# Kernel optimization log

Hardware: AMD Instinct MI355X
Metric: run time of the kernel (lower is better)

Reference implementation:

```python
import jax, jax.numpy as jnp
import numpy as np

GROUP_SIZE = 128

def setup_inputs() -> dict:
    key = jax.random.key(0)
    k1, k2, k3, k4, k5 = jax.random.split(key, 5)
    B, S, IN, OUT = 4, 2048, 4096, 4096
    G = IN // GROUP_SIZE  # 32 groups
    x = jax.random.normal(k1, (B, S, IN), dtype=jnp.float32)
    qweight = jax.random.randint(k2, (OUT, IN // 2), 0, 256, dtype=jnp.int32)
    scales = jax.random.uniform(k3, (OUT, G), dtype=jnp.float32) * 0.01 + 1e-4
    zeros = jax.random.randint(k4, (OUT, G), 0, 16, dtype=jnp.int32)
    bias = jax.random.normal(k5, (OUT,), dtype=jnp.float32) * 0.01
    return {"x": x, "qweight": qweight, "scales": scales, "zeros": zeros, "bias": bias}

def reference(x, qweight, scales, zeros, bias):
    out_f, half = qweight.shape
    in_f = half * 2
    G = scales.shape[1]
    # Unpack two 4-bit values per byte: low nibble at even index, high at odd.
    low = (qweight & 15).astype(x.dtype)
    high = ((qweight >> 4) & 15).astype(x.dtype)
    w = jnp.stack([low, high], axis=-1).reshape(out_f, in_f)  # interleaved [w0,w1,w2,...]
    # Groupwise dequant: (q - zero) * scale
    w = w.reshape(out_f, G, GROUP_SIZE)
    w = (w - zeros[:, :, None].astype(x.dtype)) * scales[:, :, None].astype(x.dtype)
    w = w.reshape(out_f, in_f)
    # Dense linear: y = x @ W^T + b
    out = jnp.einsum('bsi,oi->bso', x, w) + bias
    return out
```

## Files before the change

kernel.cpp:

```cpp
#include <hip/hip_runtime.h>
#include <hip/hip_bf16.h>

typedef __attribute__((ext_vector_type(4))) float f32x4;
typedef __attribute__((ext_vector_type(8))) short bf16x8;
typedef __attribute__((ext_vector_type(4))) int i32x4;

#define GS 128

#define GLOAD_LDS16(g, l)                                                        \
    __builtin_amdgcn_global_load_lds(                                            \
        (const __attribute__((address_space(1))) void*)(g),                      \
        (__attribute__((address_space(3))) void*)(l), 16, 0, 0)

__device__ __forceinline__ short f2bf(float f) {
    union { float f; unsigned u; } v; v.f = f;
    unsigned r = v.u + 0x7fffu + ((v.u >> 16) & 1u);
    return (short)(r >> 16);
}

__global__ void prep_kernel(const int* __restrict__ QW,
                            const float* __restrict__ SC,
                            const int* __restrict__ ZR,
                            const float* __restrict__ X,
                            signed char* __restrict__ W8,
                            float* __restrict__ WS,
                            signed char* __restrict__ Xq,
                            float* __restrict__ XS,
                            int N, int K, int G) {
    const int tid = threadIdx.x;
    const int lane = tid & 63;
    const int wid = tid >> 6;
    __shared__ float red[4];

    if ((int)blockIdx.x < N) {
        const int o = blockIdx.x;
        const int g = tid / 8;
        const float s = SC[(long)o * G + g];
        const float z = (float)ZR[(long)o * G + g];
        const int* p = QW + (long)o * (K / 2) + tid * 8;
        int v[8];
#pragma unroll
        for (int j = 0; j < 8; ++j) v[j] = p[j];
        float w[16];
#pragma unroll
        for (int j = 0; j < 8; ++j) {
            w[2 * j]     = ((float)(v[j] & 15) - z) * s;
            w[2 * j + 1] = ((float)((v[j] >> 4) & 15) - z) * s;
        }
        float am = 0.f;
#pragma unroll
        for (int j = 0; j < 16; ++j) am = fmaxf(am, fabsf(w[j]));
#pragma unroll
        for (int off = 32; off >= 1; off >>= 1) am = fmaxf(am, __shfl_xor(am, off));
        if (lane == 0) red[wid] = am;
        __syncthreads();
        float wmax = fmaxf(fmaxf(red[0], red[1]), fmaxf(red[2], red[3]));
        wmax = fmaxf(wmax, 1e-30f);
        const float qs = 127.0f / wmax;
        int out[4];
#pragma unroll
        for (int j = 0; j < 4; ++j) {
            int b0 = ((int)rintf(w[4 * j]     * qs)) & 255;
            int b1 = ((int)rintf(w[4 * j + 1] * qs)) & 255;
            int b2 = ((int)rintf(w[4 * j + 2] * qs)) & 255;
            int b3 = ((int)rintf(w[4 * j + 3] * qs)) & 255;
            out[j] = b0 | (b1 << 8) | (b2 << 16) | (b3 << 24);
        }
        *(i32x4*)(W8 + (long)o * K + tid * 16) = *(i32x4*)out;
        if (tid == 0) WS[o] = wmax / 127.0f;
    } else {
        const int row = blockIdx.x - N;
        const float* px = X + (long)row * K + tid * 16;
        f32x4 v[4];
#pragma unroll
        for (int j = 0; j < 4; ++j) v[j] = *(const f32x4*)(px + j * 4);
        float am = 0.f;
#pragma unroll
        for (int j = 0; j < 4; ++j)
#pragma unroll
            for (int i = 0; i < 4; ++i) am = fmaxf(am, fabsf(v[j][i]));
#pragma unroll
        for (int off = 32; off >= 1; off >>= 1) am = fmaxf(am, __shfl_xor(am, off));
        if (lane == 0) red[wid] = am;
        __syncthreads();
        float amax = fmaxf(fmaxf(red[0], red[1]), fmaxf(red[2], red[3]));
        amax = fmaxf(amax, 1e-30f);
        const float qs = 127.0f / amax;
        int out[4];
#pragma unroll
        for (int j = 0; j < 4; ++j) {
            int b0 = ((int)rintf(v[j][0] * qs)) & 255;
            int b1 = ((int)rintf(v[j][1] * qs)) & 255;
            int b2 = ((int)rintf(v[j][2] * qs)) & 255;
            int b3 = ((int)rintf(v[j][3] * qs)) & 255;
            out[j] = b0 | (b1 << 8) | (b2 << 16) | (b3 << 24);
        }
        *(i32x4*)(Xq + (long)row * K + tid * 16) = *(i32x4*)out;
        if (tid == 0) XS[row] = amax / 127.0f;
    }
}

__global__ __launch_bounds__(512, 2)
void gemm_i8_kernel(const signed char* __restrict__ A,
                    const signed char* __restrict__ B,
                    const float* __restrict__ WS,
                    const float* __restrict__ XS,
                    const float* __restrict__ BI,
                    float* __restrict__ Y,
                    int M, int N, int K) {
    extern __shared__ char smem[];

    const int tid = threadIdx.x;
    const int lane = tid & 63;
    const int wid = tid >> 6;
    const int wr = wid >> 2;
    const int wc = wid & 3;
    const int fr = lane & 15;
    const int fq = lane >> 4;

    const int nbn = N / 256;
    const int bid = blockIdx.x;
    const int cpx = gridDim.x >> 3;
    const int wgid = (bid & 7) * cpx + (bid >> 3);
    const int tm = wgid / nbn;
    const int tn = wgid % nbn;
    const long m0 = (long)tm * 256;
    const long n0 = (long)tn * 256;

    const int srow = wid * 8 + (lane >> 3);
    const int schunk = (lane & 7) ^ (lane >> 3);
    const signed char* gA = A + (m0 + srow) * (long)K + schunk * 16;
    const signed char* gB = B + (n0 + srow) * (long)K + schunk * 16;

    auto stageA = [&](int c2, int i, int kt) {
        GLOAD_LDS16(gA + (long)i * 64 * K + (long)kt * 128,
                    smem + c2 * 32768 + i * 8192 + wid * 1024);
    };
    auto stageB = [&](int b3, int i, int kt) {
        GLOAD_LDS16(gB + (long)i * 64 * K + (long)kt * 128,
                    smem + 65536 + b3 * 32768 + i * 8192 + wid * 1024);
    };

    const int rswz = fr & 7;

    i32x4 acc[8][4] = {};
    i32x4 bfr[4][2];
    i32x4 afr[4];

    const int NT = K / 128;

    stageB(0, 0, 0); stageB(0, 1, 0); stageB(0, 2, 0); stageB(0, 3, 0);
    stageA(0, 0, 0); stageA(0, 1, 0); stageA(0, 2, 0); stageA(0, 3, 0);
    stageB(1, 0, 1); stageB(1, 1, 1); stageB(1, 2, 1); stageB(1, 3, 1);
    asm volatile("s_waitcnt vmcnt(4)" ::: "memory");
    __builtin_amdgcn_s_barrier();

    for (int t = 0; t < NT - 2; ++t) {
        const char* sA = smem + (t & 1) * 32768;
        const char* sB = smem + 65536 + (t % 3) * 32768;
        const int nxtA = (t & 1) ^ 1;
        const int b2 = (t + 2) % 3;
#pragma unroll
        for (int ph = 0; ph < 4; ++ph) {
            const int ks = ph & 1;
            const int mh = ph >> 1;
#pragma unroll
            for (int mf = 0; mf < 4; ++mf) {
                int row = wr * 128 + mh * 64 + mf * 16 + fr;
                afr[mf] = *(const i32x4*)(sA + row * 128 + ((fq + 4 * ks) ^ rswz) * 16);
            }
            if (mh == 0) {
#pragma unroll
                for (int nf = 0; nf < 4; ++nf) {
                    int row = wc * 64 + nf * 16 + fr;
                    bfr[nf][ks] = *(const i32x4*)(sB + row * 128 + ((fq + 4 * ks) ^ rswz) * 16);
                }
            }
            if (ph == 0)      { stageA(nxtA, 0, t + 1); stageA(nxtA, 2, t + 1); }
            else if (ph == 1) { stageA(nxtA, 1, t + 1); stageA(nxtA, 3, t + 1); }
            else if (ph == 2) { stageB(b2, 0, t + 2); stageB(b2, 1, t + 2); }
            else              { stageB(b2, 2, t + 2); stageB(b2, 3, t + 2); }

            __builtin_amdgcn_s_setprio(1);
#pragma unroll
            for (int mf = 0; mf < 4; ++mf)
#pragma unroll
                for (int nf = 0; nf < 4; ++nf)
                    acc[mh * 4 + mf][nf] = __builtin_amdgcn_mfma_i32_16x16x64_i8(
                        afr[mf], bfr[nf][ks], acc[mh * 4 + mf][nf], 0, 0, 0);
            __builtin_amdgcn_s_setprio(0);
        }
        asm volatile("s_waitcnt vmcnt(4)" ::: "memory");
        __builtin_amdgcn_s_barrier();
    }

    {
        const int t = NT - 2;
        const char* sA = smem + (t & 1) * 32768;
        const char* sB = smem + 65536 + (t % 3) * 32768;
        const int nxtA = (t & 1) ^ 1;
#pragma unroll
        for (int ph = 0; ph < 4; ++ph) {
            const int ks = ph & 1;
            const int mh = ph >> 1;
#pragma unroll
            for (int mf = 0; mf < 4; ++mf) {
                int row = wr * 128 + mh * 64 + mf * 16 + fr;
                afr[mf] = *(const i32x4*)(sA + row * 128 + ((fq + 4 * ks) ^ rswz) * 16);
            }
            if (mh == 0) {
#pragma unroll
                for (int nf = 0; nf < 4; ++nf) {
                    int row = wc * 64 + nf * 16 + fr;
                    bfr[nf][ks] = *(const i32x4*)(sB + row * 128 + ((fq + 4 * ks) ^ rswz) * 16);
                }
            }
            if (ph == 0)      { stageA(nxtA, 0, t + 1); stageA(nxtA, 2, t + 1); }
            else if (ph == 1) { stageA(nxtA, 1, t + 1); stageA(nxtA, 3, t + 1); }

            __builtin_amdgcn_s_setprio(1);
#pragma unroll
            for (int mf = 0; mf < 4; ++mf)
#pragma unroll
                for (int nf = 0; nf < 4; ++nf)
                    acc[mh * 4 + mf][nf] = __builtin_amdgcn_mfma_i32_16x16x64_i8(
                        afr[mf], bfr[nf][ks], acc[mh * 4 + mf][nf], 0, 0, 0);
            __builtin_amdgcn_s_setprio(0);
        }
        asm volatile("s_waitcnt vmcnt(0)" ::: "memory");
        __builtin_amdgcn_s_barrier();
    }

    {
        const int t = NT - 1;
        const char* sA = smem + (t & 1) * 32768;
        const char* sB = smem + 65536 + (t % 3) * 32768;
#pragma unroll
        for (int ph = 0; ph < 4; ++ph) {
            const int ks = ph & 1;
            const int mh = ph >> 1;
#pragma unroll
            for (int mf = 0; mf < 4; ++mf) {
                int row = wr * 128 + mh * 64 + mf * 16 + fr;
                afr[mf] = *(const i32x4*)(sA + row * 128 + ((fq + 4 * ks) ^ rswz) * 16);
            }
            if (mh == 0) {
#pragma unroll
                for (int nf = 0; nf < 4; ++nf) {
                    int row = wc * 64 + nf * 16 + fr;
                    bfr[nf][ks] = *(const i32x4*)(sB + row * 128 + ((fq + 4 * ks) ^ rswz) * 16);
                }
            }
            __builtin_amdgcn_s_setprio(1);
#pragma unroll
            for (int mf = 0; mf < 4; ++mf)
#pragma unroll
                for (int nf = 0; nf < 4; ++nf)
                    acc[mh * 4 + mf][nf] = __builtin_amdgcn_mfma_i32_16x16x64_i8(
                        afr[mf], bfr[nf][ks], acc[mh * 4 + mf][nf], 0, 0, 0);
            __builtin_amdgcn_s_setprio(0);
        }
    }

#pragma unroll
    for (int nf = 0; nf < 4; ++nf) {
        const long col = n0 + wc * 64 + nf * 16 + fr;
        const float ws = WS[col];
        const float bv = BI[col];
#pragma unroll
        for (int m = 0; m < 8; ++m) {
            const long rbase = m0 + wr * 128 + (m >> 2) * 64 + (m & 3) * 16 + 4 * fq;
#pragma unroll
            for (int i = 0; i < 4; ++i)
                Y[(rbase + i) * N + col] =
                    (float)acc[m][nf][i] * (XS[rbase + i] * ws) + bv;
        }
    }
}

#define BM 128
#define BN 128
#define BK 64
#define PK 72

__global__ void gptq_gemm_fallback(const float* __restrict__ X,
                                   const int* __restrict__ QW,
                                   const float* __restrict__ SC,
                                   const int* __restrict__ ZR,
                                   const float* __restrict__ BI,
                                   float* __restrict__ Y,
                                   int M, int N, int K, int G) {
    __shared__ __align__(16) short As[BM * PK];
    __shared__ __align__(16) short Bs[BN * PK];

    const int tid = threadIdx.x;
    const int nbm = M / BM;
    const int bid = blockIdx.x;
    const int cpx = gridDim.x >> 3;
    const int wgid = (bid & 7) * cpx + (bid >> 3);
    const int tm = wgid % nbm;
    const int tn = wgid / nbm;
    const long m0 = (long)tm * BM;
    const long n0 = (long)tn * BN;
    const int Kp = K >> 1;

    const int lane = tid & 63;
    const int wid = tid >> 6;
    const int wr = wid >> 1;
    const int wc = wid & 1;
    const int fr = lane & 15;
    const int fq = lane >> 4;

    int srow[4], sq[4];
#pragma unroll
    for (int c = 0; c < 4; ++c) {
        int w = tid + 256 * c;
        srow[c] = w >> 3;
        sq[c] = w & 7;
    }

    f32x4 acc[4][4] = {};
    const int NT = K / BK;

    for (int kt = 0; kt < NT; ++kt) {
        const int g = (kt * BK) / GS;
        f32x4 a0[4], a1[4];
        i32x4 b4[4];
        float sc_r[4], zr_r[4];
#pragma unroll
        for (int c = 0; c < 4; ++c) {
            const float* pa = X + (m0 + srow[c]) * K + kt * BK + 8 * sq[c];
            a0[c] = *(const f32x4*)pa;
            a1[c] = *(const f32x4*)(pa + 4);
            const int* pb = QW + (n0 + srow[c]) * Kp + kt * (BK / 2) + 4 * sq[c];
            b4[c] = *(const i32x4*)pb;
            sc_r[c] = SC[(n0 + srow[c]) * G + g];
            zr_r[c] = (float)ZR[(n0 + srow[c]) * G + g];
        }
        __syncthreads();
#pragma unroll
        for (int c = 0; c < 4; ++c) {
            bf16x8 av;
#pragma unroll
            for (int i = 0; i < 4; ++i) av[i] = f2bf(a0[c][i]);
#pragma unroll
            for (int i = 0; i < 4; ++i) av[4 + i] = f2bf(a1[c][i]);
            *(bf16x8*)(As + srow[c] * PK + 8 * sq[c]) = av;
            bf16x8 bv;
#pragma unroll
            for (int j = 0; j < 4; ++j) {
                int v = b4[c][j];
                bv[2 * j]     = f2bf(((float)(v & 15) - zr_r[c]) * sc_r[c]);
                bv[2 * j + 1] = f2bf(((float)((v >> 4) & 15) - zr_r[c]) * sc_r[c]);
            }
            *(bf16x8*)(Bs + srow[c] * PK + 8 * sq[c]) = bv;
        }
        __syncthreads();
#pragma unroll
        for (int kk = 0; kk < BK; kk += 32) {
            bf16x8 a[4], b[4];
#pragma unroll
            for (int mf = 0; mf < 4; ++mf)
                a[mf] = *(const bf16x8*)(As + (wr * 64 + mf * 16 + fr) * PK + kk + 8 * fq);
#pragma unroll
            for (int nf = 0; nf < 4; ++nf)
                b[nf] = *(const bf16x8*)(Bs + (wc * 64 + nf * 16 + fr) * PK + kk + 8 * fq);
#pragma unroll
            for (int mf = 0; mf < 4; ++mf)
#pragma unroll
                for (int nf = 0; nf < 4; ++nf)
                    acc[mf][nf] = __builtin_amdgcn_mfma_f32_16x16x32_bf16(
                        a[mf], b[nf], acc[mf][nf], 0, 0, 0);
        }
    }

#pragma unroll
    for (int nf = 0; nf < 4; ++nf) {
        const long col = n0 + wc * 64 + nf * 16 + fr;
        const float bias_v = BI[col];
#pragma unroll
        for (int mf = 0; mf < 4; ++mf) {
            const long rbase = m0 + wr * 64 + mf * 16 + 4 * fq;
#pragma unroll
            for (int i = 0; i < 4; ++i)
                Y[(rbase + i) * N + col] = acc[mf][nf][i] + bias_v;
        }
    }
}

extern "C" void kernel_launch(void* const* d_in, const int* in_sizes, int n_in,
                              void* d_out, int out_size, void* d_ws, size_t ws_size,
                              hipStream_t stream) {
    const float* X = (const float*)d_in[0];
    const int* QW = (const int*)d_in[1];
    const float* SC = (const float*)d_in[2];
    const int* ZR = (const int*)d_in[3];
    const float* BI = (const float*)d_in[4];
    float* Y = (float*)d_out;

    const int N = in_sizes[4];
    const int G = in_sizes[2] / N;
    const int K = G * GS;
    const int M = in_sizes[0] / K;

    const size_t needW8 = (size_t)N * K;
    const size_t needXq = (size_t)M * K;
    const size_t needXS = (size_t)M * 4;
    const size_t needWS = (size_t)N * 4;
    const size_t need = needW8 + needXq + needXS + needWS;

    if (ws_size >= need) {
        signed char* W8 = (signed char*)d_ws;
        signed char* Xq = W8 + needW8;
        float* XS = (float*)(Xq + needXq);
        float* WS = XS + M;

        hipLaunchKernelGGL(prep_kernel, dim3(N + M), dim3(256), 0, stream,
                           QW, SC, ZR, X, W8, WS, Xq, XS, N, K, G);

        (void)hipFuncSetAttribute((const void*)gemm_i8_kernel,
                                  hipFuncAttributeMaxDynamicSharedMemorySize, 163840);
        const int grid = (M / 256) * (N / 256);
        hipLaunchKernelGGL(gemm_i8_kernel, dim3(grid), dim3(512), 163840, stream,
                           Xq, W8, WS, XS, BI, Y, M, N, K);
    } else {
        const int grid = (M / BM) * (N / BN);
        hipLaunchKernelGGL(gptq_gemm_fallback, dim3(grid), dim3(256), 0, stream,
                           X, QW, SC, ZR, BI, Y, M, N, K, G);
    }
}
```

Before: 179.3 us.

## Shrink int8 GEMM tile to 128x128 with four waves per block

Reduces the int8 GEMM block tile from 256x256 (8 waves) to 128x128 (4 waves) and halves shared memory to 80KB. Staging, LDS offsets, fragment loops and the epilogue are restructured so each wave owns a 64x64 sub-tile, and each k-step now issues all A stages, then all B stages. This gives four times as many blocks and lets more blocks fit on each CU, improving tail balance across CUs. In exchange each block reuses its loaded data less, so more global and LDS traffic is needed per MFMA.

```diff
diff --git a/kernel.cpp b/kernel.cpp
--- a/kernel.cpp
+++ b/kernel.cpp
@@ -100,7 +100,7 @@
     }
 }
 
-__global__ __launch_bounds__(512, 2)
+__global__ __launch_bounds__(256, 2)
 void gemm_i8_kernel(const signed char* __restrict__ A,
                     const signed char* __restrict__ B,
                     const float* __restrict__ WS,
@@ -113,19 +113,19 @@
     const int tid = threadIdx.x;
     const int lane = tid & 63;
     const int wid = tid >> 6;
-    const int wr = wid >> 2;
-    const int wc = wid & 3;
+    const int wr = wid >> 1;
+    const int wc = wid & 1;
     const int fr = lane & 15;
     const int fq = lane >> 4;
 
-    const int nbn = N / 256;
+    const int nbn = N / 128;
     const int bid = blockIdx.x;
     const int cpx = gridDim.x >> 3;
     const int wgid = (bid & 7) * cpx + (bid >> 3);
     const int tm = wgid / nbn;
     const int tn = wgid % nbn;
-    const long m0 = (long)tm * 256;
-    const long n0 = (long)tn * 256;
+    const long m0 = (long)tm * 128;
+    const long n0 = (long)tn * 128;
 
     const int srow = wid * 8 + (lane >> 3);
     const int schunk = (lane & 7) ^ (lane >> 3);
@@ -133,19 +133,18 @@
     const signed char* gB = B + (n0 + srow) * (long)K + schunk * 16;
 
     auto stageA = [&](int c2, int i, int kt) {
-        GLOAD_LDS16(gA + (long)i * 64 * K + (long)kt * 128,
-                    smem + c2 * 32768 + i * 8192 + wid * 1024);
+        GLOAD_LDS16(gA + (long)i * 32 * K + (long)kt * 128,
+                    smem + c2 * 16384 + i * 4096 + wid * 1024);
     };
     auto stageB = [&](int b3, int i, int kt) {
-        GLOAD_LDS16(gB + (long)i * 64 * K + (long)kt * 128,
-                    smem + 65536 + b3 * 32768 + i * 8192 + wid * 1024);
+        GLOAD_LDS16(gB + (long)i * 32 * K + (long)kt * 128,
+                    smem + 32768 + b3 * 16384 + i * 4096 + wid * 1024);
     };
 
     const int rswz = fr & 7;
 
-    i32x4 acc[8][4] = {};
-    i32x4 bfr[4][2];
-    i32x4 afr[4];
+    i32x4 acc[4][4] = {};
+    i32x4 afr[4], bfr[4];
 
     const int NT = K / 128;
 
@@ -156,38 +155,34 @@
     __builtin_amdgcn_s_barrier();
 
     for (int t = 0; t < NT - 2; ++t) {
-        const char* sA = smem + (t & 1) * 32768;
-        const char* sB = smem + 65536 + (t % 3) * 32768;
+        const char* sA = smem + (t & 1) * 16384;
+        const char* sB = smem + 32768 + (t % 3) * 16384;
         const int nxtA = (t & 1) ^ 1;
         const int b2 = (t + 2) % 3;
 #pragma unroll
-        for (int ph = 0; ph < 4; ++ph) {
-            const int ks = ph & 1;
-            const int mh = ph >> 1;
+        for (int ks = 0; ks < 2; ++ks) {
 #pragma unroll
             for (int mf = 0; mf < 4; ++mf) {
-                int row = wr * 128 + mh * 64 + mf * 16 + fr;
+                int row = wr * 64 + mf * 16 + fr;
                 afr[mf] = *(const i32x4*)(sA + row * 128 + ((fq + 4 * ks) ^ rswz) * 16);
             }
-            if (mh == 0) {
-#pragma unroll
-                for (int nf = 0; nf < 4; ++nf) {
-                    int row = wc * 64 + nf * 16 + fr;
-                    bfr[nf][ks] = *(const i32x4*)(sB + row * 128 + ((fq + 4 * ks) ^ rswz) * 16);
-                }
-            }
-            if (ph == 0)      { stageA(nxtA, 0, t + 1); stageA(nxtA, 2, t + 1); }
-            else if (ph == 1) { stageA(nxtA, 1, t + 1); stageA(nxtA, 3, t + 1); }
-            else if (ph == 2) { stageB(b2, 0, t + 2); stageB(b2, 1, t + 2); }
-            else              { stageB(b2, 2, t + 2); stageB(b2, 3, t + 2); }
+#pragma unroll
+            for (int nf = 0; nf < 4; ++nf) {
+                int row = wc * 64 + nf * 16 + fr;
+                bfr[nf] = *(const i32x4*)(sB + row * 128 + ((fq + 4 * ks) ^ rswz) * 16);
+            }
+            if (ks == 0) { stageA(nxtA, 0, t + 1); stageA(nxtA, 1, t + 1);
+                           stageA(nxtA, 2, t + 1); stageA(nxtA, 3, t + 1); }
+            else         { stageB(b2, 0, t + 2); stageB(b2, 1, t + 2);
+                           stageB(b2, 2, t + 2); stageB(b2, 3, t + 2); }
 
             __builtin_amdgcn_s_setprio(1);
 #pragma unroll
             for (int mf = 0; mf < 4; ++mf)
 #pragma unroll
                 for (int nf = 0; nf < 4; ++nf)
-                    acc[mh * 4 + mf][nf] = __builtin_amdgcn_mfma_i32_16x16x64_i8(
-                        afr[mf], bfr[nf][ks], acc[mh * 4 + mf][nf], 0, 0, 0);
+                    acc[mf][nf] = __builtin_amdgcn_mfma_i32_16x16x64_i8(
+                        afr[mf], bfr[nf], acc[mf][nf], 0, 0, 0);
             __builtin_amdgcn_s_setprio(0);
         }
         asm volatile("s_waitcnt vmcnt(4)" ::: "memory");
@@ -196,35 +191,31 @@
 
     {
         const int t = NT - 2;
-        const char* sA = smem + (t & 1) * 32768;
-        const char* sB = smem + 65536 + (t % 3) * 32768;
+        const char* sA = smem + (t & 1) * 16384;
+        const char* sB = smem + 32768 + (t % 3) * 16384;
         const int nxtA = (t & 1) ^ 1;
 #pragma unroll
-        for (int ph = 0; ph < 4; ++ph) {
-            const int ks = ph & 1;
-            const int mh = ph >> 1;
+        for (int ks = 0; ks < 2; ++ks) {
 #pragma unroll
             for (int mf = 0; mf < 4; ++mf) {
-                int row = wr * 128 + mh * 64 + mf * 16 + fr;
+                int row = wr * 64 + mf * 16 + fr;
                 afr[mf] = *(const i32x4*)(sA + row * 128 + ((fq + 4 * ks) ^ rswz) * 16);
             }
-            if (mh == 0) {
-#pragma unroll
-                for (int nf = 0; nf < 4; ++nf) {
-                    int row = wc * 64 + nf * 16 + fr;
-                    bfr[nf][ks] = *(const i32x4*)(sB + row * 128 + ((fq + 4 * ks) ^ rswz) * 16);
-                }
-            }
-            if (ph == 0)      { stageA(nxtA, 0, t + 1); stageA(nxtA, 2, t + 1); }
-            else if (ph == 1) { stageA(nxtA, 1, t + 1); stageA(nxtA, 3, t + 1); }
+#pragma unroll
+            for (int nf = 0; nf < 4; ++nf) {
+                int row = wc * 64 + nf * 16 + fr;
+                bfr[nf] = *(const i32x4*)(sB + row * 128 + ((fq + 4 * ks) ^ rswz) * 16);
+            }
+            if (ks == 0) { stageA(nxtA, 0, t + 1); stageA(nxtA, 1, t + 1);
+                           stageA(nxtA, 2, t + 1); stageA(nxtA, 3, t + 1); }
 
             __builtin_amdgcn_s_setprio(1);
 #pragma unroll
             for (int mf = 0; mf < 4; ++mf)
 #pragma unroll
                 for (int nf = 0; nf < 4; ++nf)
-                    acc[mh * 4 + mf][nf] = __builtin_amdgcn_mfma_i32_16x16x64_i8(
-                        afr[mf], bfr[nf][ks], acc[mh * 4 + mf][nf], 0, 0, 0);
+                    acc[mf][nf] = __builtin_amdgcn_mfma_i32_16x16x64_i8(
+                        afr[mf], bfr[nf], acc[mf][nf], 0, 0, 0);
             __builtin_amdgcn_s_setprio(0);
         }
         asm volatile("s_waitcnt vmcnt(0)" ::: "memory");
@@ -233,31 +224,27 @@
 
     {
         const int t = NT - 1;
-        const char* sA = smem + (t & 1) * 32768;
-        const char* sB = smem + 65536 + (t % 3) * 32768;
-#pragma unroll
-        for (int ph = 0; ph < 4; ++ph) {
-            const int ks = ph & 1;
-            const int mh = ph >> 1;
+        const char* sA = smem + (t & 1) * 16384;
+        const char* sB = smem + 32768 + (t % 3) * 16384;
+#pragma unroll
+        for (int ks = 0; ks < 2; ++ks) {
 #pragma unroll
             for (int mf = 0; mf < 4; ++mf) {
-                int row = wr * 128 + mh * 64 + mf * 16 + fr;
+                int row = wr * 64 + mf * 16 + fr;
                 afr[mf] = *(const i32x4*)(sA + row * 128 + ((fq + 4 * ks) ^ rswz) * 16);
             }
-            if (mh == 0) {
-#pragma unroll
-                for (int nf = 0; nf < 4; ++nf) {
-                    int row = wc * 64 + nf * 16 + fr;
-                    bfr[nf][ks] = *(const i32x4*)(sB + row * 128 + ((fq + 4 * ks) ^ rswz) * 16);
-                }
+#pragma unroll
+            for (int nf = 0; nf < 4; ++nf) {
+                int row = wc * 64 + nf * 16 + fr;
+                bfr[nf] = *(const i32x4*)(sB + row * 128 + ((fq + 4 * ks) ^ rswz) * 16);
             }
             __builtin_amdgcn_s_setprio(1);
 #pragma unroll
             for (int mf = 0; mf < 4; ++mf)
 #pragma unroll
                 for (int nf = 0; nf < 4; ++nf)
-                    acc[mh * 4 + mf][nf] = __builtin_amdgcn_mfma_i32_16x16x64_i8(
-                        afr[mf], bfr[nf][ks], acc[mh * 4 + mf][nf], 0, 0, 0);
+                    acc[mf][nf] = __builtin_amdgcn_mfma_i32_16x16x64_i8(
+                        afr[mf], bfr[nf], acc[mf][nf], 0, 0, 0);
             __builtin_amdgcn_s_setprio(0);
         }
     }
@@ -268,12 +255,12 @@
         const float ws = WS[col];
         const float bv = BI[col];
 #pragma unroll
-        for (int m = 0; m < 8; ++m) {
-            const long rbase = m0 + wr * 128 + (m >> 2) * 64 + (m & 3) * 16 + 4 * fq;
+        for (int mf = 0; mf < 4; ++mf) {
+            const long rbase = m0 + wr * 64 + mf * 16 + 4 * fq;
 #pragma unroll
             for (int i = 0; i < 4; ++i)
                 Y[(rbase + i) * N + col] =
-                    (float)acc[m][nf][i] * (XS[rbase + i] * ws) + bv;
+                    (float)acc[mf][nf][i] * (XS[rbase + i] * ws) + bv;
         }
     }
 }
@@ -419,9 +406,9 @@
                            QW, SC, ZR, X, W8, WS, Xq, XS, N, K, G);
 
         (void)hipFuncSetAttribute((const void*)gemm_i8_kernel,
-                                  hipFuncAttributeMaxDynamicSharedMemorySize, 163840);
-        const int grid = (M / 256) * (N / 256);
-        hipLaunchKernelGGL(gemm_i8_kernel, dim3(grid), dim3(512), 163840, stream,
+                                  hipFuncAttributeMaxDynamicSharedMemorySize, 81920);
+        const int grid = (M / 128) * (N / 128);
+        hipLaunchKernelGGL(gemm_i8_kernel, dim3(grid), dim3(256), 81920, stream,
                            Xq, W8, WS, XS, BI, Y, M, N, K);
     } else {
         const int grid = (M / BM) * (N / BN);
```

Measured after the change: 219.7 us. 1.23x slower.
